# Optimization experiments

Hardware: AMD Instinct MI355X
Metric: run time of the kernel (lower is better)

## Reference

```python
import jax, jax.numpy as jnp
import numpy as np
import math

EMBED_DIM = 1024
HEAD_DIM = 64
BATCH = 4
SEQ = 4096


def setup_inputs() -> dict:
    key = jax.random.key(0)
    k1, k2 = jax.random.split(key)
    x = jax.random.normal(k1, (BATCH, SEQ, EMBED_DIM), dtype=jnp.float32)
    QKV = jax.random.normal(k2, (EMBED_DIM, 3 * HEAD_DIM), dtype=jnp.float32) * (1.0 / math.sqrt(EMBED_DIM))
    return {"x": x, "QKV": QKV}


def reference(x, QKV):
    head_dim = QKV.shape[-1] // 3
    scale = 1.0 / math.sqrt(head_dim)
    qkv = x @ QKV                      # [b, s, 3*d]
    q, k, v = jnp.split(qkv, 3, axis=-1)
    scores = jnp.einsum('bqd,bkd->bqk', q, k) * scale  # [b, s, s]
    weights = jax.nn.softmax(scores, axis=-1)
    out = jnp.einsum('bqk,bkd->bqd', weights, v)        # [b, s, d]
    return out
```

## Files before the change

### kernel.cpp

```cpp
#include <hip/hip_runtime.h>
#include <hip/hip_bf16.h>

#define BATCH 4
#define SEQ   4096
#define EMB   1024
#define HD    64
#define N3    192
#define NSPLIT 8

typedef __attribute__((ext_vector_type(8)))  short short8;
typedef __attribute__((ext_vector_type(4)))  float floatx4;
typedef __attribute__((ext_vector_type(16))) float floatx16;
typedef unsigned long long ull;
typedef unsigned short us;

#define SSCALE 0.1803368801111204f

static __device__ __forceinline__ us f2bf(float f) {
    unsigned int u = __float_as_uint(f);
    u += 0x7fffu + ((u >> 16) & 1u);
    return (us)(u >> 16);
}
static __device__ __forceinline__ float bf2f(us h) {
    return __uint_as_float((unsigned int)h << 16);
}
static __device__ __forceinline__ unsigned int cvtpk(float lo, float hi) {
    unsigned int r;
    asm("v_cvt_pk_bf16_f32 %0, %1, %2" : "=v"(r) : "v"(lo), "v"(hi));
    return r;
}
static __device__ __forceinline__ void gll16(const void* g, void* l) {
    __builtin_amdgcn_global_load_lds(
        (const __attribute__((address_space(1))) unsigned int*)(unsigned long long)g,
        (__attribute__((address_space(3))) unsigned int*)(unsigned int)(unsigned long long)l,
        16, 0, 0);
}

#define MFMA16(A, B, C) __builtin_amdgcn_mfma_f32_16x16x32_bf16(A, B, C, 0, 0, 0)
#define MFMA32(A, B, C) __builtin_amdgcn_mfma_f32_32x32x16_bf16(A, B, C, 0, 0, 0)

__global__ __launch_bounds__(256) void wt_prep(const float* __restrict__ w,
                                               us* __restrict__ wf)
{
    int t = blockIdx.x * 256 + threadIdx.x;
    int l  = t & 63;
    int cb = (t >> 6) % 12;
    int kb = t / (64 * 12);
    int kbase = kb * 32 + (l >> 4) * 8;
    int n = cb * 16 + (l & 15);
    us e[8];
#pragma unroll
    for (int i = 0; i < 8; ++i)
        e[i] = f2bf(w[(size_t)(kbase + i) * N3 + n]);
    *(short8*)(wf + (size_t)t * 8) = *(short8*)e;
}

__global__ __launch_bounds__(1024, 4) void qkv_proj(
    const float* __restrict__ x, const us* __restrict__ wf,
    us* __restrict__ q, us* __restrict__ k, us* __restrict__ vt)
{
    const int tid = threadIdx.x;
    const int w   = tid >> 6;
    const int l   = tid & 63;
    const int ln  = l & 15;
    const int g   = l >> 4;
    const int wm  = w >> 2;
    const int wn  = w & 3;
    const int row0 = blockIdx.x * 64;

    __shared__ __align__(16) char Xs[2][32768];

    auto stage = [&](int c) {
#pragma unroll
        for (int i = 0; i < 2; ++i) {
            int unit = i * 1024 + tid;
            int row  = unit >> 5;
            int su   = unit & 31;
            gll16(x + (size_t)(row0 + row) * EMB + c * 128 + ((su ^ (row & 7)) << 2),
                  Xs[c & 1] + unit * 16);
        }
    };

    stage(0);

    floatx4 acc[3];
#pragma unroll
    for (int ng = 0; ng < 3; ++ng) acc[ng] = (floatx4){0.f, 0.f, 0.f, 0.f};

    const int rowl = wm * 16 + ln;

    for (int c = 0; c < 8; ++c) {
        asm volatile("s_waitcnt vmcnt(0)" ::: "memory");
        __builtin_amdgcn_sched_barrier(0);
        __syncthreads();

        short8 wfr[4][3];
#pragma unroll
        for (int ks = 0; ks < 4; ++ks)
#pragma unroll
            for (int ng = 0; ng < 3; ++ng)
                wfr[ks][ng] = *(const short8*)(wf +
                    ((size_t)((c * 4 + ks) * 12 + wn * 3 + ng) * 64 + l) * 8);
        asm volatile("" ::: "memory");

        if (c < 7) stage(c + 1);

        const char* Bx = Xs[c & 1];
#pragma unroll
        for (int ks = 0; ks < 4; ++ks) {
            int ub = ks * 8 + g * 2;
            float4 a0 = *(const float4*)(Bx + rowl * 512 + (((ub + 0) ^ (rowl & 7)) << 4));
            float4 a1 = *(const float4*)(Bx + rowl * 512 + (((ub + 1) ^ (rowl & 7)) << 4));
            unsigned int p0 = cvtpk(a0.x, a0.y), p1 = cvtpk(a0.z, a0.w);
            unsigned int p2 = cvtpk(a1.x, a1.y), p3 = cvtpk(a1.z, a1.w);
            int4 av = {(int)p0, (int)p1, (int)p2, (int)p3};
            short8 af = *(short8*)&av;
#pragma unroll
            for (int ng = 0; ng < 3; ++ng)
                acc[ng] = MFMA16(af, wfr[ks][ng], acc[ng]);
        }
    }

#pragma unroll
    for (int ng = 0; ng < 3; ++ng) {
        int n = wn * 48 + ng * 16 + ln;
#pragma unroll
        for (int j = 0; j < 4; ++j) {
            int grow = row0 + wm * 16 + g * 4 + j;
            int b = grow >> 12;
            int s = grow & 4095;
            if (n < 64)
                q[(size_t)(b * SEQ + s) * HD + n] = f2bf(acc[ng][j] * SSCALE);
            else if (n < 128)
                k[(size_t)(b * SEQ + s) * HD + (n - 64)] = f2bf(acc[ng][j]);
            else
                vt[((size_t)b * HD + (n - 128)) * SEQ + s] = f2bf(acc[ng][j]);
        }
    }
}

__global__ __launch_bounds__(512, 4) void attn(
    const us* __restrict__ qg, const us* __restrict__ kg,
    const us* __restrict__ vtg, us* __restrict__ pob, float* __restrict__ pml)
{
    const int tid = threadIdx.x;
    const int w   = tid >> 6;
    const int l   = tid & 63;
    const int qn  = l & 31;
    const int u   = l >> 5;
    const int bid = blockIdx.x;
    const int split = bid & 7;
    const int qt  = (bid >> 3) & 15;
    const int b   = bid >> 7;
    const int qr0 = qt * 256 + w * 32;

    __shared__ __align__(16) char LDSbuf[32768];

    const us* kbase = kg  + (size_t)b * SEQ * HD;
    const us* vbase = vtg + (size_t)b * HD * SEQ;

    const us* qrow = qg + ((size_t)(b * SEQ) + qr0 + qn) * HD;
    short8 qf[4];
#pragma unroll
    for (int t = 0; t < 4; ++t) qf[t] = *(const short8*)(qrow + t * 16 + u * 8);

    const int ktbase = split * 8;

    auto stage = [&](int ktg, char* Kd, char* Vd) {
        int row = tid >> 3;
        int c16 = (tid & 7) ^ (row & 7);
        gll16(kbase + (size_t)(ktg * 64 + row) * HD + c16 * 8, Kd + tid * 16);
        gll16(vbase + (size_t)row * SEQ + ktg * 64 + c16 * 8, Vd + tid * 16);
    };

    stage(ktbase, LDSbuf, LDSbuf + 8192);

    floatx16 o0 = {}, o1 = {};
    float m_run = -1e30f, l_run = 0.f;

    for (int kt = 0; kt < 8; ++kt) {
        asm volatile("s_waitcnt vmcnt(0)" ::: "memory");
        __syncthreads();
        char* Ks = LDSbuf + (kt & 1) * 16384;
        char* Vs = Ks + 8192;
        if (kt < 7) {
            char* Kn = LDSbuf + ((kt + 1) & 1) * 16384;
            stage(ktbase + kt + 1, Kn, Kn + 8192);
        }

        floatx16 sa0 = {}, sa1 = {};
        __builtin_amdgcn_s_setprio(1);
#pragma unroll
        for (int t = 0; t < 4; ++t) {
            int r0 = qn, r1 = 32 + qn;
            short8 kf0 = *(const short8*)(Ks + r0 * 128 + ((32 * t + 16 * u) ^ ((r0 & 7) << 4)));
            short8 kf1 = *(const short8*)(Ks + r1 * 128 + ((32 * t + 16 * u) ^ ((r1 & 7) << 4)));
            sa0 = MFMA32(kf0, qf[t], sa0);
            sa1 = MFMA32(kf1, qf[t], sa1);
        }
        __builtin_amdgcn_s_setprio(0);

        float red[16];
#pragma unroll
        for (int r = 0; r < 16; ++r) red[r] = fmaxf(sa0[r], sa1[r]);
#pragma unroll
        for (int s = 8; s > 0; s >>= 1)
#pragma unroll
            for (int r = 0; r < s; ++r) red[r] = fmaxf(red[r], red[r + s]);
        float tm = fmaxf(red[0], __shfl_xor(red[0], 32));

        if (!__all(tm <= m_run + 8.f)) {
            float mn  = fmaxf(m_run, tm);
            float fac = exp2f(m_run - mn);
            m_run = mn;
            l_run *= fac;
#pragma unroll
            for (int r = 0; r < 16; ++r) { o0[r] *= fac; o1[r] *= fac; }
        }
#pragma unroll
        for (int r = 0; r < 16; ++r) { sa0[r] = exp2f(sa0[r] - m_run); }
#pragma unroll
        for (int r = 0; r < 16; ++r) { sa1[r] = exp2f(sa1[r] - m_run); }
        float sred[16];
#pragma unroll
        for (int r = 0; r < 16; ++r) sred[r] = sa0[r] + sa1[r];
#pragma unroll
        for (int s = 8; s > 0; s >>= 1)
#pragma unroll
            for (int r = 0; r < s; ++r) sred[r] += sred[r + s];
        l_run += sred[0] + __shfl_xor(sred[0], 32);

        __builtin_amdgcn_s_setprio(1);
#pragma unroll
        for (int s = 0; s < 4; ++s) {
            unsigned int A0, A1, B0, B1;
            if (s == 0) {
                A0 = cvtpk(sa0[0], sa0[1]);  A1 = cvtpk(sa0[2], sa0[3]);
                B0 = cvtpk(sa0[4], sa0[5]);  B1 = cvtpk(sa0[6], sa0[7]);
            } else if (s == 1) {
                A0 = cvtpk(sa0[8], sa0[9]);  A1 = cvtpk(sa0[10], sa0[11]);
                B0 = cvtpk(sa0[12], sa0[13]); B1 = cvtpk(sa0[14], sa0[15]);
            } else if (s == 2) {
                A0 = cvtpk(sa1[0], sa1[1]);  A1 = cvtpk(sa1[2], sa1[3]);
                B0 = cvtpk(sa1[4], sa1[5]);  B1 = cvtpk(sa1[6], sa1[7]);
            } else {
                A0 = cvtpk(sa1[8], sa1[9]);  A1 = cvtpk(sa1[10], sa1[11]);
                B0 = cvtpk(sa1[12], sa1[13]); B1 = cvtpk(sa1[14], sa1[15]);
            }
            asm("v_permlane32_swap_b32 %0, %1" : "+v"(A0), "+v"(B0));
            asm("v_permlane32_swap_b32 %0, %1" : "+v"(A1), "+v"(B1));
            int4 pbv = {(int)A0, (int)A1, (int)B0, (int)B1};
            short8 pb = *(short8*)&pbv;

            int rv0 = qn, rv1 = 32 + qn;
            short8 vf0 = *(const short8*)(Vs + rv0 * 128 + ((32 * s + 16 * u) ^ ((rv0 & 7) << 4)));
            short8 vf1 = *(const short8*)(Vs + rv1 * 128 + ((32 * s + 16 * u) ^ ((rv1 & 7) << 4)));
            o0 = MFMA32(vf0, pb, o0);
            o1 = MFMA32(vf1, pb, o1);
        }
        __builtin_amdgcn_s_setprio(0);
    }

    const size_t prow0 = (size_t)split * (BATCH * SEQ) + (size_t)b * SEQ + qr0;
    float* Ts = (float*)(LDSbuf + (w & 3) * 8192);
#pragma unroll
    for (int round = 0; round < 2; ++round) {
        __syncthreads();
        if ((w >> 2) == round) {
#pragma unroll
            for (int r = 0; r < 16; ++r) {
                int d = (r & 3) + 8 * (r >> 2) + 4 * u;
                Ts[d * 32 + qn]        = o0[r];
                Ts[(d + 32) * 32 + qn] = o1[r];
            }
#pragma unroll
            for (int c = 0; c < 8; ++c) {
                float v0 = Ts[(u * 32 + c * 4 + 0) * 32 + qn];
                float v1 = Ts[(u * 32 + c * 4 + 1) * 32 + qn];
                float v2 = Ts[(u * 32 + c * 4 + 2) * 32 + qn];
                float v3 = Ts[(u * 32 + c * 4 + 3) * 32 + qn];
                ull pk =  (ull)f2bf(v0) | ((ull)f2bf(v1) << 16)
                       | ((ull)f2bf(v2) << 32) | ((ull)f2bf(v3) << 48);
                *(ull*)(pob + (prow0 + qn) * HD + u * 32 + c * 4) = pk;
            }
        }
    }
    if (l < 32) {
        pml[(prow0 + l) * 2 + 0] = m_run;
        pml[(prow0 + l) * 2 + 1] = l_run;
    }
}

__global__ __launch_bounds__(256) void recombine(
    const us* __restrict__ pob, const float* __restrict__ pml,
    float* __restrict__ out)
{
    int idx = blockIdx.x * 256 + threadIdx.x;
    int row = idx >> 3;
    int c8  = idx & 7;

    float m[NSPLIT], lv[NSPLIT];
#pragma unroll
    for (int i = 0; i < NSPLIT; ++i) {
        m[i]  = pml[((size_t)i * (BATCH * SEQ) + row) * 2 + 0];
        lv[i] = pml[((size_t)i * (BATCH * SEQ) + row) * 2 + 1];
    }
    float M = m[0];
#pragma unroll
    for (int i = 1; i < NSPLIT; ++i) M = fmaxf(M, m[i]);
    float wt[NSPLIT], denom = 0.f;
#pragma unroll
    for (int i = 0; i < NSPLIT; ++i) { wt[i] = exp2f(m[i] - M); denom += wt[i] * lv[i]; }
    float inv = 1.0f / denom;

    float acc[8];
#pragma unroll
    for (int e = 0; e < 8; ++e) acc[e] = 0.f;
#pragma unroll
    for (int i = 0; i < NSPLIT; ++i) {
        short8 v = *(const short8*)(pob + ((size_t)i * (BATCH * SEQ) + row) * HD + c8 * 8);
#pragma unroll
        for (int e = 0; e < 8; ++e) acc[e] += wt[i] * bf2f((us)v[e]);
    }
    float4 r0 = {acc[0] * inv, acc[1] * inv, acc[2] * inv, acc[3] * inv};
    float4 r1 = {acc[4] * inv, acc[5] * inv, acc[6] * inv, acc[7] * inv};
    *(float4*)(out + (size_t)row * HD + c8 * 8)     = r0;
    *(float4*)(out + (size_t)row * HD + c8 * 8 + 4) = r1;
}

extern "C" void kernel_launch(void* const* d_in, const int* in_sizes, int n_in,
                              void* d_out, int out_size, void* d_ws, size_t ws_size,
                              hipStream_t stream) {
    (void)in_sizes; (void)n_in; (void)out_size; (void)ws_size;
    const float* x = (const float*)d_in[0];
    const float* w = (const float*)d_in[1];
    float* out = (float*)d_out;

    const size_t QE = (size_t)BATCH * SEQ * HD;
    us* q   = (us*)d_ws;
    us* k   = q + QE;
    us* vt  = k + QE;
    us* wfb = vt + QE;
    us* pob = wfb + (size_t)N3 * EMB;
    float* pml = (float*)(pob + (size_t)NSPLIT * BATCH * SEQ * HD);

    wt_prep  <<<dim3(96),   dim3(256),  0, stream>>>(w, wfb);
    qkv_proj <<<dim3(256),  dim3(1024), 0, stream>>>(x, wfb, q, k, vt);
    attn     <<<dim3(512),  dim3(512),  0, stream>>>(q, k, vt, pob, pml);
    recombine<<<dim3(512),  dim3(256),  0, stream>>>(pob, pml, out);
}
```

Measured before the change: 157.7 us.

## Triple-buffer LDS staging in projection and attention, halve projection block size

The QKV projection kernel now uses 512-thread blocks covering 32 rows each and twice as many blocks. Both it and the attention kernel switch from double to triple-buffered global-to-LDS staging, prefetching two tiles ahead with partial vmcnt waits. The attention kernel also issues its K/V prefetch before the Q fragment loads, and issues the next stage right after the barrier. The aim is to hide more global-load latency and add parallelism for the projection, at the cost of more LDS per block in attention (48KB), which may lower occupancy.

```diff
diff --git a/kernel.cpp b/kernel.cpp
--- a/kernel.cpp
+++ b/kernel.cpp
@@ -55,7 +55,7 @@
     *(short8*)(wf + (size_t)t * 8) = *(short8*)e;
 }
 
-__global__ __launch_bounds__(1024, 4) void qkv_proj(
+__global__ __launch_bounds__(512, 4) void qkv_proj(
     const float* __restrict__ x, const us* __restrict__ wf,
     us* __restrict__ q, us* __restrict__ k, us* __restrict__ vt)
 {
@@ -66,22 +66,25 @@
     const int g   = l >> 4;
     const int wm  = w >> 2;
     const int wn  = w & 3;
-    const int row0 = blockIdx.x * 64;
-
-    __shared__ __align__(16) char Xs[2][32768];
+    const int row0 = blockIdx.x * 32;
+
+    __shared__ __align__(16) char Xs[3][16384];
+
+    const int srow  = tid >> 5;
+    const int sunit = tid & 31;
 
     auto stage = [&](int c) {
+        char* dst = Xs[c % 3];
 #pragma unroll
         for (int i = 0; i < 2; ++i) {
-            int unit = i * 1024 + tid;
-            int row  = unit >> 5;
-            int su   = unit & 31;
-            gll16(x + (size_t)(row0 + row) * EMB + c * 128 + ((su ^ (row & 7)) << 2),
-                  Xs[c & 1] + unit * 16);
+            int row = i * 16 + srow;
+            gll16(x + (size_t)(row0 + row) * EMB + c * 128 + ((sunit ^ (row & 7)) << 2),
+                  dst + i * 8192 + tid * 16);
         }
     };
 
     stage(0);
+    stage(1);
 
     floatx4 acc[3];
 #pragma unroll
@@ -90,7 +93,8 @@
     const int rowl = wm * 16 + ln;
 
     for (int c = 0; c < 8; ++c) {
-        asm volatile("s_waitcnt vmcnt(0)" ::: "memory");
+        if (c < 7) asm volatile("s_waitcnt vmcnt(2)" ::: "memory");
+        else       asm volatile("s_waitcnt vmcnt(0)" ::: "memory");
         __builtin_amdgcn_sched_barrier(0);
         __syncthreads();
 
@@ -103,9 +107,9 @@
                     ((size_t)((c * 4 + ks) * 12 + wn * 3 + ng) * 64 + l) * 8);
         asm volatile("" ::: "memory");
 
-        if (c < 7) stage(c + 1);
-
-        const char* Bx = Xs[c & 1];
+        if (c < 6) stage(c + 2);
+
+        const char* Bx = Xs[c % 3];
 #pragma unroll
         for (int ks = 0; ks < 4; ++ks) {
             int ub = ks * 8 + g * 2;
@@ -154,39 +158,40 @@
     const int b   = bid >> 7;
     const int qr0 = qt * 256 + w * 32;
 
-    __shared__ __align__(16) char LDSbuf[32768];
+    __shared__ __align__(16) char LDSbuf[49152];
 
     const us* kbase = kg  + (size_t)b * SEQ * HD;
     const us* vbase = vtg + (size_t)b * HD * SEQ;
 
-    const us* qrow = qg + ((size_t)(b * SEQ) + qr0 + qn) * HD;
-    short8 qf[4];
-#pragma unroll
-    for (int t = 0; t < 4; ++t) qf[t] = *(const short8*)(qrow + t * 16 + u * 8);
-
     const int ktbase = split * 8;
 
-    auto stage = [&](int ktg, char* Kd, char* Vd) {
+    auto stage = [&](int ktg, int buf) {
+        char* Kd = LDSbuf + buf * 16384;
         int row = tid >> 3;
         int c16 = (tid & 7) ^ (row & 7);
         gll16(kbase + (size_t)(ktg * 64 + row) * HD + c16 * 8, Kd + tid * 16);
-        gll16(vbase + (size_t)row * SEQ + ktg * 64 + c16 * 8, Vd + tid * 16);
+        gll16(vbase + (size_t)row * SEQ + ktg * 64 + c16 * 8, Kd + 8192 + tid * 16);
     };
 
-    stage(ktbase, LDSbuf, LDSbuf + 8192);
+    stage(ktbase + 0, 0);
+    stage(ktbase + 1, 1);
+
+    const us* qrow = qg + ((size_t)(b * SEQ) + qr0 + qn) * HD;
+    short8 qf[4];
+#pragma unroll
+    for (int t = 0; t < 4; ++t) qf[t] = *(const short8*)(qrow + t * 16 + u * 8);
 
     floatx16 o0 = {}, o1 = {};
     float m_run = -1e30f, l_run = 0.f;
 
     for (int kt = 0; kt < 8; ++kt) {
-        asm volatile("s_waitcnt vmcnt(0)" ::: "memory");
+        if (kt < 7) asm volatile("s_waitcnt vmcnt(2)" ::: "memory");
+        else        asm volatile("s_waitcnt vmcnt(0)" ::: "memory");
+        __builtin_amdgcn_sched_barrier(0);
         __syncthreads();
-        char* Ks = LDSbuf + (kt & 1) * 16384;
+        if (kt < 6) stage(ktbase + kt + 2, (kt + 2) % 3);
+        char* Ks = LDSbuf + (kt % 3) * 16384;
         char* Vs = Ks + 8192;
-        if (kt < 7) {
-            char* Kn = LDSbuf + ((kt + 1) & 1) * 16384;
-            stage(ktbase + kt + 1, Kn, Kn + 8192);
-        }
 
         floatx16 sa0 = {}, sa1 = {};
         __builtin_amdgcn_s_setprio(1);
@@ -344,8 +349,8 @@
     us* pob = wfb + (size_t)N3 * EMB;
     float* pml = (float*)(pob + (size_t)NSPLIT * BATCH * SEQ * HD);
 
-    wt_prep  <<<dim3(96),   dim3(256),  0, stream>>>(w, wfb);
-    qkv_proj <<<dim3(256),  dim3(1024), 0, stream>>>(x, wfb, q, k, vt);
-    attn     <<<dim3(512),  dim3(512),  0, stream>>>(q, k, vt, pob, pml);
-    recombine<<<dim3(512),  dim3(256),  0, stream>>>(pob, pml, out);
-}
+    wt_prep  <<<dim3(96),   dim3(256), 0, stream>>>(w, wfb);
+    qkv_proj <<<dim3(512),  dim3(512), 0, stream>>>(x, wfb, q, k, vt);
+    attn     <<<dim3(512),  dim3(512), 0, stream>>>(q, k, vt, pob, pml);
+    recombine<<<dim3(512),  dim3(256), 0, stream>>>(pob, pml, out);
+}
```

After: 149.0 us. 5.5% less time.
